# Kernel tuning notes

Hardware: AMD Instinct MI355X
Metric: run time of the kernel (lower is better)

## Reference

```python
import jax, jax.numpy as jnp
import numpy as np

N_NODES = 50000
N_EDGES = 800000
IN_C, HID_C, OUT_C = 256, 256, 128


def gcn_conv(x, W, b, row, col, n_nodes):
    """PyG GCNConv: linear transform, symmetric-normalized aggregation, bias.
    row/col already include self-loops. Messages flow row -> col."""
    h = x @ W  # [N, out]
    deg = jax.ops.segment_sum(jnp.ones_like(col, dtype=h.dtype), col, num_segments=n_nodes)
    d_inv_sqrt = jnp.where(deg > 0, jax.lax.rsqrt(jnp.maximum(deg, 1e-12)), 0.0)
    norm = d_inv_sqrt[row] * d_inv_sqrt[col]  # [E]
    msg = h[row] * norm[:, None]              # gather + scale, [E, out]
    out = jax.ops.segment_sum(msg, col, num_segments=n_nodes)  # scatter-add
    return out + b


def setup_inputs() -> dict:
    key = jax.random.key(0)
    k_x, k_e, k_w1, k_w2 = jax.random.split(key, 4)
    x = jax.random.normal(k_x, (N_NODES, IN_C), dtype=jnp.float32)
    edge_index = jax.random.randint(k_e, (2, N_EDGES), 0, N_NODES, dtype=jnp.int64)
    # Glorot-style init for GCN weights, zeros bias (PyG default)
    s1 = float(np.sqrt(6.0 / (IN_C + HID_C)))
    s2 = float(np.sqrt(6.0 / (HID_C + OUT_C)))
    W1 = jax.random.uniform(k_w1, (IN_C, HID_C), dtype=jnp.float32, minval=-s1, maxval=s1)
    b1 = jnp.zeros((HID_C,), dtype=jnp.float32)
    W2 = jax.random.uniform(k_w2, (HID_C, OUT_C), dtype=jnp.float32, minval=-s2, maxval=s2)
    b2 = jnp.zeros((OUT_C,), dtype=jnp.float32)
    return {"x": x, "edge_index": edge_index, "W1": W1, "b1": b1, "W2": W2, "b2": b2}


def reference(x, edge_index, W1, b1, W2, b2):
    n = x.shape[0]
    # add self-loops (PyG GCNConv default add_self_loops=True)
    loops = jnp.arange(n, dtype=edge_index.dtype)
    row = jnp.concatenate([edge_index[0], loops])
    col = jnp.concatenate([edge_index[1], loops])
    h = gcn_conv(x, W1, b1, row, col, n)
    h = jax.nn.relu(h)  # dropout p=0.0 -> identity
    out = gcn_conv(h, W2, b2, row, col, n)
    return out
```

## Files before the change

### kernel.cpp

```cpp
#include <hip/hip_runtime.h>

#define NN 50000
#define NE 800000
#define IN_C 256
#define HID_C 256
#define OUT_C 128

typedef unsigned short u16;
typedef __attribute__((ext_vector_type(8))) short short8;
typedef __attribute__((ext_vector_type(8))) unsigned short ushort8;
typedef __attribute__((ext_vector_type(4))) float f32x4;

__device__ __forceinline__ u16 f2b(float f) {
  unsigned int u = __float_as_uint(f);
  return (u16)((u + 0x7FFFu + ((u >> 16) & 1u)) >> 16);
}
__device__ __forceinline__ float b2f(u16 s) {
  return __uint_as_float(((unsigned int)s) << 16);
}


__global__ __launch_bounds__(256) void convw_hist(const float* __restrict__ W1,
                                                  const float* __restrict__ W2,
                                                  u16* __restrict__ W1t,
                                                  u16* __restrict__ W2t,
                                                  const int* __restrict__ col,
                                                  int* __restrict__ cnt, int E, int nhb) {
  int b = blockIdx.x;
  if (b < 256) {
    int id = b * 256 + threadIdx.x;
    int n = id >> 8, k = id & 255;
    W1t[id] = f2b(W1[k * 256 + n]);
    if (id < 128 * 256) W2t[id] = f2b(W2[k * 128 + n]);
  } else {
    int T = nhb * 256;
    int idx = (b - 256) * 256 + threadIdx.x;
#pragma unroll
    for (int i = 0; i < 8; ++i) {
      int e = idx + i * T;
      if (e < E) atomicAdd(&cnt[col[e]], 1);
    }
  }
}


__global__ __launch_bounds__(256) void scan1_kernel(const int* __restrict__ cnt,
                                                    int* __restrict__ bsum, int n) {
  __shared__ int ws[4];
  int i = blockIdx.x * 256 + threadIdx.x;
  int lane = threadIdx.x & 63, wid = threadIdx.x >> 6;
  int v = (i < n) ? cnt[i] : 0;
#pragma unroll
  for (int off = 32; off > 0; off >>= 1) v += __shfl_down(v, off, 64);
  if (lane == 0) ws[wid] = v;
  __syncthreads();
  if (threadIdx.x == 0) bsum[blockIdx.x] = ws[0] + ws[1] + ws[2] + ws[3];
}

__global__ __launch_bounds__(256) void scan23_kernel(const int* __restrict__ cnt,
                                                     const int* __restrict__ bsum,
                                                     int* __restrict__ row_off,
                                                     int* __restrict__ cursor,
                                                     float* __restrict__ dinv, int n) {
  __shared__ int ws2[4];
  __shared__ int wsum[4], wpre[4];
  int bid = blockIdx.x;
  int t = threadIdx.x;
  int lane = t & 63, wid = t >> 6;
  int bv = (t < bid) ? bsum[t] : 0;
#pragma unroll
  for (int off = 32; off > 0; off >>= 1) bv += __shfl_down(bv, off, 64);
  if (lane == 0) ws2[wid] = bv;
  __syncthreads();
  int boff = ws2[0] + ws2[1] + ws2[2] + ws2[3];
  int i = bid * 256 + t;
  int v = (i < n) ? cnt[i] : 0;
  int s = v;
#pragma unroll
  for (int off = 1; off < 64; off <<= 1) {
    int tt = __shfl_up(s, off, 64);
    if (lane >= off) s += tt;
  }
  if (lane == 63) wsum[wid] = s;
  __syncthreads();
  if (t == 0) {
    int acc = 0;
#pragma unroll
    for (int w = 0; w < 4; ++w) { wpre[w] = acc; acc += wsum[w]; }
  }
  __syncthreads();
  if (i < n) {
    int off = boff + wpre[wid] + (s - v);
    row_off[i] = off;
    cursor[i] = off;
    dinv[i] = rsqrtf((float)(v + 1));
  }
  if (bid == 0 && t == 0) row_off[n] = NE;
}


template <bool A_IS_F32>
__device__ __forceinline__ void gemm_body(const void* __restrict__ Ap,
                                          const u16* __restrict__ Bt,
                                          const float* __restrict__ dscale,
                                          u16* __restrict__ C, int M, int N,
                                          int bx, int by,
                                          u16 (&Asl)[2][5120], u16 (&Bsl)[2][5120]) {
  const int tid = threadIdx.x;
  const int row0 = by * 128;
  const int col0 = bx * 128;

  f32x4 acc[4][4] = {};

  const int seg = tid & 7;
  const int rb = tid >> 3;
  const int wave = tid >> 6, lane = tid & 63;
  const int wm = wave >> 1, wn = wave & 1;
  const int qr = lane & 15, quad = lane >> 4;

  float4 aF[4];
  ushort4 aU[4];
  ushort4 bR[4];

  auto load_tiles = [&](int k0) {
    if constexpr (A_IS_F32) {
      const float* A = (const float*)Ap;
#pragma unroll
      for (int i = 0; i < 4; ++i) {
        int gr = row0 + rb + i * 32;
        aF[i] = (gr < M) ? *(const float4*)&A[(size_t)gr * 256 + k0 + seg * 4]
                         : make_float4(0.f, 0.f, 0.f, 0.f);
      }
    } else {
      const u16* A = (const u16*)Ap;
#pragma unroll
      for (int i = 0; i < 4; ++i) {
        int gr = row0 + rb + i * 32;
        aU[i] = (gr < M) ? *(const ushort4*)&A[(size_t)gr * 256 + k0 + seg * 4]
                         : make_ushort4(0, 0, 0, 0);
      }
    }
#pragma unroll
    for (int i = 0; i < 4; ++i) {
      int n = rb + i * 32;
      bR[i] = *(const ushort4*)&Bt[(size_t)(col0 + n) * 256 + k0 + seg * 4];
    }
  };

  auto write_lds = [&](int buf) {
#pragma unroll
    for (int i = 0; i < 4; ++i) {
      int r = rb + i * 32;
      ushort4 u;
      if constexpr (A_IS_F32) {
        u.x = f2b(aF[i].x); u.y = f2b(aF[i].y);
        u.z = f2b(aF[i].z); u.w = f2b(aF[i].w);
      } else {
        u = aU[i];
      }
      *(ushort4*)&Asl[buf][r * 40 + seg * 4] = u;
      *(ushort4*)&Bsl[buf][r * 40 + seg * 4] = bR[i];
    }
  };

  load_tiles(0);
  write_lds(0);
  __syncthreads();

#pragma unroll
  for (int it = 0; it < 8; ++it) {
    const int cur = it & 1;
    if (it < 7) load_tiles((it + 1) * 32);

    short8 afr[4], bfr[4];
#pragma unroll
    for (int mt = 0; mt < 4; ++mt)
      afr[mt] = *(const short8*)&Asl[cur][(wm * 64 + mt * 16 + qr) * 40 + quad * 8];
#pragma unroll
    for (int nt = 0; nt < 4; ++nt)
      bfr[nt] = *(const short8*)&Bsl[cur][(wn * 64 + nt * 16 + qr) * 40 + quad * 8];
#pragma unroll
    for (int mt = 0; mt < 4; ++mt)
#pragma unroll
      for (int nt = 0; nt < 4; ++nt)
        acc[mt][nt] = __builtin_amdgcn_mfma_f32_16x16x32_bf16(afr[mt], bfr[nt], acc[mt][nt], 0, 0, 0);

    if (it < 7) {
      write_lds(1 - cur);
      __syncthreads();
    }
  }

#pragma unroll
  for (int mt = 0; mt < 4; ++mt) {
#pragma unroll
    for (int i = 0; i < 4; ++i) {
      int gr = row0 + wm * 64 + mt * 16 + quad * 4 + i;
      if (gr < M) {
        float sc = dscale[gr];
#pragma unroll
        for (int nt = 0; nt < 4; ++nt) {
          int gc = col0 + wn * 64 + nt * 16 + qr;
          C[(size_t)gr * N + gc] = f2b(acc[mt][nt][i] * sc);
        }
      }
    }
  }
}

template <bool A_IS_F32>
__global__ __launch_bounds__(256) void gemm_mfma(const void* __restrict__ Ap,
                                                 const u16* __restrict__ Bt,
                                                 const float* __restrict__ dscale,
                                                 u16* __restrict__ C, int M, int N) {
  __shared__ u16 Asl[2][5120];
  __shared__ u16 Bsl[2][5120];
  gemm_body<A_IS_F32>(Ap, Bt, dscale, C, M, N, blockIdx.x, blockIdx.y, Asl, Bsl);
}

__global__ __launch_bounds__(256) void gemm1_scatter(const float* __restrict__ x,
                                                     const u16* __restrict__ W1t,
                                                     const float* __restrict__ dinv,
                                                     u16* __restrict__ Hb, int M, int N,
                                                     int ngb,
                                                     const int* __restrict__ row,
                                                     const int* __restrict__ col,
                                                     int* __restrict__ cursor,
                                                     int* __restrict__ csr, int E, int nsb) {
  __shared__ u16 Asl[2][5120];
  __shared__ u16 Bsl[2][5120];
  int b = blockIdx.x;
  if (b < ngb) {
    gemm_body<true>(x, W1t, dinv, Hb, M, N, b & 1, b >> 1, Asl, Bsl);
  } else {
    int T = nsb * 256;
    int idx = (b - ngb) * 256 + threadIdx.x;
#pragma unroll
    for (int i = 0; i < 8; ++i) {
      int e = idx + i * T;
      if (e < E) {
        int c = col[e];
        int p = atomicAdd(&cursor[c], 1);
        csr[p] = row[e];
      }
    }
  }
}


__global__ __launch_bounds__(256) void agg256_bf(const u16* __restrict__ h,
                                                 const int* __restrict__ row_off,
                                                 const int* __restrict__ csr,
                                                 const float* __restrict__ dinv,
                                                 const float* __restrict__ bias,
                                                 u16* __restrict__ out, int n) {
  int wave = threadIdx.x >> 6;
  int lane = threadIdx.x & 63;
  int half = lane >> 5;
  int sl = lane & 31;
  int v = blockIdx.x * 8 + wave * 2 + half;
  if (v >= n) return;
  int beg = row_off[v], end = row_off[v + 1];
  float a[8] = {};
  int e = beg;
  for (; e < end && (e & 3); ++e) {
    int s0 = csr[e];
    ushort8 g0 = *(const ushort8*)&h[(size_t)s0 * 256 + sl * 8];
#pragma unroll
    for (int i = 0; i < 8; ++i) a[i] += b2f((u16)g0[i]);
  }
  for (; e + 7 < end; e += 8) {
    int4 i0 = *(const int4*)&csr[e];
    int4 i1 = *(const int4*)&csr[e + 4];
    int s[8] = {i0.x, i0.y, i0.z, i0.w, i1.x, i1.y, i1.z, i1.w};
    ushort8 g[8];
#pragma unroll
    for (int j = 0; j < 8; ++j)
      g[j] = *(const ushort8*)&h[(size_t)s[j] * 256 + sl * 8];
#pragma unroll
    for (int j = 0; j < 8; ++j)
#pragma unroll
      for (int i = 0; i < 8; ++i) a[i] += b2f((u16)g[j][i]);
  }
  for (; e < end; ++e) {
    int s0 = csr[e];
    ushort8 g0 = *(const ushort8*)&h[(size_t)s0 * 256 + sl * 8];
#pragma unroll
    for (int i = 0; i < 8; ++i) a[i] += b2f((u16)g0[i]);
  }
  ushort8 hs = *(const ushort8*)&h[(size_t)v * 256 + sl * 8];
#pragma unroll
  for (int i = 0; i < 8; ++i) a[i] += b2f((u16)hs[i]);
  float dv = dinv[v];
  float4 bv0 = *(const float4*)&bias[sl * 8];
  float4 bv1 = *(const float4*)&bias[sl * 8 + 4];
  float bb[8] = {bv0.x, bv0.y, bv0.z, bv0.w, bv1.x, bv1.y, bv1.z, bv1.w};
  ushort8 o;
#pragma unroll
  for (int i = 0; i < 8; ++i) {
    float r = fmaxf(a[i] * dv + bb[i], 0.f);
    o[i] = (short)f2b(r);
  }
  *(ushort8*)&out[(size_t)v * 256 + sl * 8] = o;
}

__global__ __launch_bounds__(256) void agg128_bf(const u16* __restrict__ h,
                                                 const int* __restrict__ row_off,
                                                 const int* __restrict__ csr,
                                                 const float* __restrict__ dinv,
                                                 const float* __restrict__ bias,
                                                 float* __restrict__ out, int n) {
  int wave = threadIdx.x >> 6;
  int lane = threadIdx.x & 63;
  int quarter = lane >> 4;
  int sl = lane & 15;
  int v = blockIdx.x * 16 + wave * 4 + quarter;
  if (v >= n) return;
  int beg = row_off[v], end = row_off[v + 1];
  float a[8] = {};
  int e = beg;
  for (; e < end && (e & 3); ++e) {
    int s0 = csr[e];
    ushort8 g0 = *(const ushort8*)&h[(size_t)s0 * 128 + sl * 8];
#pragma unroll
    for (int i = 0; i < 8; ++i) a[i] += b2f((u16)g0[i]);
  }
  for (; e + 7 < end; e += 8) {
    int4 i0 = *(const int4*)&csr[e];
    int4 i1 = *(const int4*)&csr[e + 4];
    int s[8] = {i0.x, i0.y, i0.z, i0.w, i1.x, i1.y, i1.z, i1.w};
    ushort8 g[8];
#pragma unroll
    for (int j = 0; j < 8; ++j)
      g[j] = *(const ushort8*)&h[(size_t)s[j] * 128 + sl * 8];
#pragma unroll
    for (int j = 0; j < 8; ++j)
#pragma unroll
      for (int i = 0; i < 8; ++i) a[i] += b2f((u16)g[j][i]);
  }
  for (; e < end; ++e) {
    int s0 = csr[e];
    ushort8 g0 = *(const ushort8*)&h[(size_t)s0 * 128 + sl * 8];
#pragma unroll
    for (int i = 0; i < 8; ++i) a[i] += b2f((u16)g0[i]);
  }
  ushort8 hs = *(const ushort8*)&h[(size_t)v * 128 + sl * 8];
#pragma unroll
  for (int i = 0; i < 8; ++i) a[i] += b2f((u16)hs[i]);
  float dv = dinv[v];
  float4 bv0 = *(const float4*)&bias[sl * 8];
  float4 bv1 = *(const float4*)&bias[sl * 8 + 4];
  float bb[8] = {bv0.x, bv0.y, bv0.z, bv0.w, bv1.x, bv1.y, bv1.z, bv1.w};
  float o[8];
#pragma unroll
  for (int i = 0; i < 8; ++i) o[i] = a[i] * dv + bb[i];
  *(float4*)&out[(size_t)v * 128 + sl * 8] = make_float4(o[0], o[1], o[2], o[3]);
  *(float4*)&out[(size_t)v * 128 + sl * 8 + 4] = make_float4(o[4], o[5], o[6], o[7]);
}


extern "C" void kernel_launch(void* const* d_in, const int* in_sizes, int n_in,
                              void* d_out, int out_size, void* d_ws, size_t ws_size,
                              hipStream_t stream) {
  const float* x = (const float*)d_in[0];
  const int* ei = (const int*)d_in[1];
  const float* W1 = (const float*)d_in[2];
  const float* b1 = (const float*)d_in[3];
  const float* W2 = (const float*)d_in[4];
  const float* b2 = (const float*)d_in[5];
  float* out = (float*)d_out;

  const int* row = ei;
  const int* col = ei + NE;

  const int NB = (NN + 255) / 256;

  u16* Hb = (u16*)d_ws;
  u16* H2b = Hb + (size_t)NN * 256;
  u16* H3b = H2b + (size_t)NN * 256;
  u16* W1t = H3b + (size_t)NN * 128;
  u16* W2t = W1t + 256 * 256;
  int* cnt = (int*)(W2t + 128 * 256);
  int* row_off = cnt + NN;
  int* cursor = row_off + NN + 4;
  float* dinv = (float*)(cursor + NN);
  int* bsum = (int*)(dinv + NN);
  int* boff_unused = bsum + 200;
  int* csr = boff_unused + 200;

  hipMemsetAsync(cnt, 0, NN * sizeof(int), stream);

  {
    const int nhb = (NE + 8 * 256 - 1) / (8 * 256);
    convw_hist<<<256 + nhb, 256, 0, stream>>>(W1, W2, W1t, W2t, col, cnt, NE, nhb);
  }

  scan1_kernel<<<NB, 256, 0, stream>>>(cnt, bsum, NN);
  scan23_kernel<<<NB, 256, 0, stream>>>(cnt, bsum, row_off, cursor, dinv, NN);

  {
    const int ngb = (HID_C / 128) * ((NN + 127) / 128);
    const int nsb = (NE + 8 * 256 - 1) / (8 * 256);
    gemm1_scatter<<<ngb + nsb, 256, 0, stream>>>(x, W1t, dinv, Hb, NN, HID_C, ngb,
                                                 row, col, cursor, csr, NE, nsb);
  }

  agg256_bf<<<(NN + 7) / 8, 256, 0, stream>>>(Hb, row_off, csr, dinv, b1, H2b, NN);

  {
    dim3 grid(OUT_C / 128, (NN + 127) / 128);
    gemm_mfma<false><<<grid, 256, 0, stream>>>(H2b, W2t, dinv, H3b, NN, OUT_C);
  }
  agg128_bf<<<(NN + 15) / 16, 256, 0, stream>>>(H3b, row_off, csr, dinv, b2, out, NN);
}
```

Before: 304.1 us.

## Fuse graph setup kernels using inter-block atomic gates instead of separate launches

Replaces the memset, histogram, two scan kernels and the GEMM1/scatter launch with two kernels. Inside each, blocks coordinate through release/acquire flag gates: counter zeroing gates the histogram, block sums gate the prefix scan, and the scan gates the CSR scatter. GEMM1 now computes its row scale directly from the degree counts, so it no longer depends on the scan. This removes kernel launch gaps and serialization, but the gates are never reset between calls, so a later call can pass them early and race. It also relies on producer blocks being scheduled before the blocks that spin on them.

```diff
diff --git a/kernel.cpp b/kernel.cpp
--- a/kernel.cpp
+++ b/kernel.cpp
@@ -5,6 +5,9 @@
 #define IN_C 256
 #define HID_C 256
 #define OUT_C 128
+#define NB 196
+#define NEB 391
+#define MAGIC 0x5EED5EED
 
 typedef unsigned short u16;
 typedef __attribute__((ext_vector_type(8))) short short8;
@@ -19,90 +22,53 @@
   return __uint_as_float(((unsigned int)s) << 16);
 }
 
-
-__global__ __launch_bounds__(256) void convw_hist(const float* __restrict__ W1,
-                                                  const float* __restrict__ W2,
-                                                  u16* __restrict__ W1t,
-                                                  u16* __restrict__ W2t,
-                                                  const int* __restrict__ col,
-                                                  int* __restrict__ cnt, int E, int nhb) {
+__device__ __forceinline__ void gate_set(int* g) {
+  __hip_atomic_store(g, MAGIC, __ATOMIC_RELEASE, __HIP_MEMORY_SCOPE_AGENT);
+}
+__device__ __forceinline__ void gate_wait(const int* g) {
+  while (__hip_atomic_load(g, __ATOMIC_ACQUIRE, __HIP_MEMORY_SCOPE_AGENT) != MAGIC) {}
+}
+
+
+__global__ __launch_bounds__(256) void k1_setup(const float* __restrict__ W1,
+                                                const float* __restrict__ W2,
+                                                u16* __restrict__ W1t,
+                                                u16* __restrict__ W2t,
+                                                const int* __restrict__ col,
+                                                int* __restrict__ cnt,
+                                                int* __restrict__ zgate) {
   int b = blockIdx.x;
+  int t = threadIdx.x;
   if (b < 256) {
-    int id = b * 256 + threadIdx.x;
+    int id = b * 256 + t;
     int n = id >> 8, k = id & 255;
     W1t[id] = f2b(W1[k * 256 + n]);
     if (id < 128 * 256) W2t[id] = f2b(W2[k * 128 + n]);
+  } else if (b < 256 + NB) {
+    int sb = b - 256;
+    int i = sb * 256 + t;
+    if (i < NN) cnt[i] = 0;
+    __threadfence();
+    __syncthreads();
+    if (t == 0) gate_set(&zgate[sb]);
   } else {
-    int T = nhb * 256;
-    int idx = (b - 256) * 256 + threadIdx.x;
+    if (t < NB) gate_wait(&zgate[t]);
+    __syncthreads();
+    const int T = NEB * 256;
+    int idx = (b - 256 - NB) * 256 + t;
 #pragma unroll
     for (int i = 0; i < 8; ++i) {
       int e = idx + i * T;
-      if (e < E) atomicAdd(&cnt[col[e]], 1);
-    }
-  }
-}
-
-
-__global__ __launch_bounds__(256) void scan1_kernel(const int* __restrict__ cnt,
-                                                    int* __restrict__ bsum, int n) {
-  __shared__ int ws[4];
-  int i = blockIdx.x * 256 + threadIdx.x;
-  int lane = threadIdx.x & 63, wid = threadIdx.x >> 6;
-  int v = (i < n) ? cnt[i] : 0;
-#pragma unroll
-  for (int off = 32; off > 0; off >>= 1) v += __shfl_down(v, off, 64);
-  if (lane == 0) ws[wid] = v;
-  __syncthreads();
-  if (threadIdx.x == 0) bsum[blockIdx.x] = ws[0] + ws[1] + ws[2] + ws[3];
-}
-
-__global__ __launch_bounds__(256) void scan23_kernel(const int* __restrict__ cnt,
-                                                     const int* __restrict__ bsum,
-                                                     int* __restrict__ row_off,
-                                                     int* __restrict__ cursor,
-                                                     float* __restrict__ dinv, int n) {
-  __shared__ int ws2[4];
-  __shared__ int wsum[4], wpre[4];
-  int bid = blockIdx.x;
-  int t = threadIdx.x;
-  int lane = t & 63, wid = t >> 6;
-  int bv = (t < bid) ? bsum[t] : 0;
-#pragma unroll
-  for (int off = 32; off > 0; off >>= 1) bv += __shfl_down(bv, off, 64);
-  if (lane == 0) ws2[wid] = bv;
-  __syncthreads();
-  int boff = ws2[0] + ws2[1] + ws2[2] + ws2[3];
-  int i = bid * 256 + t;
-  int v = (i < n) ? cnt[i] : 0;
-  int s = v;
-#pragma unroll
-  for (int off = 1; off < 64; off <<= 1) {
-    int tt = __shfl_up(s, off, 64);
-    if (lane >= off) s += tt;
-  }
-  if (lane == 63) wsum[wid] = s;
-  __syncthreads();
-  if (t == 0) {
-    int acc = 0;
-#pragma unroll
-    for (int w = 0; w < 4; ++w) { wpre[w] = acc; acc += wsum[w]; }
-  }
-  __syncthreads();
-  if (i < n) {
-    int off = boff + wpre[wid] + (s - v);
-    row_off[i] = off;
-    cursor[i] = off;
-    dinv[i] = rsqrtf((float)(v + 1));
-  }
-  if (bid == 0 && t == 0) row_off[n] = NE;
-}
-
-
-template <bool A_IS_F32>
+      if (e < NE) atomicAdd(&cnt[col[e]], 1);
+    }
+  }
+}
+
+
+template <bool A_IS_F32, bool SCALE_FROM_CNT>
 __device__ __forceinline__ void gemm_body(const void* __restrict__ Ap,
                                           const u16* __restrict__ Bt,
-                                          const float* __restrict__ dscale,
+                                          const void* __restrict__ scale_src,
                                           u16* __restrict__ C, int M, int N,
                                           int bx, int by,
                                           u16 (&Asl)[2][5120], u16 (&Bsl)[2][5120]) {
@@ -197,7 +163,11 @@
     for (int i = 0; i < 4; ++i) {
       int gr = row0 + wm * 64 + mt * 16 + quad * 4 + i;
       if (gr < M) {
-        float sc = dscale[gr];
+        float sc;
+        if constexpr (SCALE_FROM_CNT)
+          sc = rsqrtf((float)(((const int*)scale_src)[gr] + 1));
+        else
+          sc = ((const float*)scale_src)[gr];
 #pragma unroll
         for (int nt = 0; nt < 4; ++nt) {
           int gc = col0 + wn * 64 + nt * 16 + qr;
@@ -208,43 +178,89 @@
   }
 }
 
-template <bool A_IS_F32>
-__global__ __launch_bounds__(256) void gemm_mfma(const void* __restrict__ Ap,
-                                                 const u16* __restrict__ Bt,
-                                                 const float* __restrict__ dscale,
-                                                 u16* __restrict__ C, int M, int N) {
-  __shared__ u16 Asl[2][5120];
-  __shared__ u16 Bsl[2][5120];
-  gemm_body<A_IS_F32>(Ap, Bt, dscale, C, M, N, blockIdx.x, blockIdx.y, Asl, Bsl);
-}
-
-__global__ __launch_bounds__(256) void gemm1_scatter(const float* __restrict__ x,
-                                                     const u16* __restrict__ W1t,
-                                                     const float* __restrict__ dinv,
-                                                     u16* __restrict__ Hb, int M, int N,
-                                                     int ngb,
-                                                     const int* __restrict__ row,
-                                                     const int* __restrict__ col,
-                                                     int* __restrict__ cursor,
-                                                     int* __restrict__ csr, int E, int nsb) {
+
+__global__ __launch_bounds__(256) void k2_scan_scatter_gemm1(
+    const int* __restrict__ cnt, int* __restrict__ bsum, int* __restrict__ sgate,
+    int* __restrict__ row_off, int* __restrict__ cursor, float* __restrict__ dinv,
+    int* __restrict__ cgate, const int* __restrict__ row, const int* __restrict__ col,
+    int* __restrict__ csr, const float* __restrict__ x, const u16* __restrict__ W1t,
+    u16* __restrict__ Hb) {
   __shared__ u16 Asl[2][5120];
   __shared__ u16 Bsl[2][5120];
   int b = blockIdx.x;
-  if (b < ngb) {
-    gemm_body<true>(x, W1t, dinv, Hb, M, N, b & 1, b >> 1, Asl, Bsl);
-  } else {
-    int T = nsb * 256;
-    int idx = (b - ngb) * 256 + threadIdx.x;
+  int t = threadIdx.x;
+  if (b < NB) {
+    __shared__ int wsum[4], wpre[5], ws2[4];
+    int lane = t & 63, wid = t >> 6;
+    int i = b * 256 + t;
+    int v = (i < NN) ? cnt[i] : 0;
+    int s = v;
+#pragma unroll
+    for (int off = 1; off < 64; off <<= 1) {
+      int tt = __shfl_up(s, off, 64);
+      if (lane >= off) s += tt;
+    }
+    if (lane == 63) wsum[wid] = s;
+    __syncthreads();
+    if (t == 0) {
+      int acc = 0;
+#pragma unroll
+      for (int w = 0; w < 4; ++w) { wpre[w] = acc; acc += wsum[w]; }
+      wpre[4] = acc;
+    }
+    __syncthreads();
+    if (t == 0) {
+      bsum[b] = wpre[4];
+      __threadfence();
+      gate_set(&sgate[b]);
+    }
+    int bv = 0;
+    if (t < b) {
+      gate_wait(&sgate[t]);
+      bv = bsum[t];
+    }
+#pragma unroll
+    for (int off = 32; off > 0; off >>= 1) bv += __shfl_down(bv, off, 64);
+    if (lane == 0) ws2[wid] = bv;
+    __syncthreads();
+    int boffs = ws2[0] + ws2[1] + ws2[2] + ws2[3];
+    if (i < NN) {
+      int off = boffs + wpre[wid] + (s - v);
+      row_off[i] = off;
+      cursor[i] = off;
+      dinv[i] = rsqrtf((float)(v + 1));
+    }
+    if (b == 0 && t == 0) row_off[NN] = NE;
+    __threadfence();
+    __syncthreads();
+    if (t == 0) gate_set(&cgate[b]);
+  } else if (b < NB + NEB) {
+    if (t < NB) gate_wait(&cgate[t]);
+    __syncthreads();
+    const int T = NEB * 256;
+    int idx = (b - NB) * 256 + t;
 #pragma unroll
     for (int i = 0; i < 8; ++i) {
       int e = idx + i * T;
-      if (e < E) {
+      if (e < NE) {
         int c = col[e];
         int p = atomicAdd(&cursor[c], 1);
-        csr[p] = row[e];
+        __builtin_nontemporal_store(row[e], &csr[p]);
       }
     }
-  }
+  } else {
+    int gb = b - NB - NEB;
+    gemm_body<true, true>(x, W1t, cnt, Hb, NN, HID_C, gb & 1, gb >> 1, Asl, Bsl);
+  }
+}
+
+__global__ __launch_bounds__(256) void gemm_mfma2(const u16* __restrict__ Ap,
+                                                  const u16* __restrict__ Bt,
+                                                  const float* __restrict__ dinv,
+                                                  u16* __restrict__ C, int M, int N) {
+  __shared__ u16 Asl[2][5120];
+  __shared__ u16 Bsl[2][5120];
+  gemm_body<false, false>(Ap, Bt, dinv, C, M, N, blockIdx.x, blockIdx.y, Asl, Bsl);
 }
 
 
@@ -373,8 +389,6 @@
   const int* row = ei;
   const int* col = ei + NE;
 
-  const int NB = (NN + 255) / 256;
-
   u16* Hb = (u16*)d_ws;
   u16* H2b = Hb + (size_t)NN * 256;
   u16* H3b = H2b + (size_t)NN * 256;
@@ -385,31 +399,22 @@
   int* cursor = row_off + NN + 4;
   float* dinv = (float*)(cursor + NN);
   int* bsum = (int*)(dinv + NN);
-  int* boff_unused = bsum + 200;
-  int* csr = boff_unused + 200;
-
-  hipMemsetAsync(cnt, 0, NN * sizeof(int), stream);
-
-  {
-    const int nhb = (NE + 8 * 256 - 1) / (8 * 256);
-    convw_hist<<<256 + nhb, 256, 0, stream>>>(W1, W2, W1t, W2t, col, cnt, NE, nhb);
-  }
-
-  scan1_kernel<<<NB, 256, 0, stream>>>(cnt, bsum, NN);
-  scan23_kernel<<<NB, 256, 0, stream>>>(cnt, bsum, row_off, cursor, dinv, NN);
-
-  {
-    const int ngb = (HID_C / 128) * ((NN + 127) / 128);
-    const int nsb = (NE + 8 * 256 - 1) / (8 * 256);
-    gemm1_scatter<<<ngb + nsb, 256, 0, stream>>>(x, W1t, dinv, Hb, NN, HID_C, ngb,
-                                                 row, col, cursor, csr, NE, nsb);
-  }
+  int* zgate = bsum + 256;
+  int* sgate = zgate + 256;
+  int* cgate = sgate + 256;
+  int* csr = cgate + 256;
+
+  k1_setup<<<256 + NB + NEB, 256, 0, stream>>>(W1, W2, W1t, W2t, col, cnt, zgate);
+
+  k2_scan_scatter_gemm1<<<NB + NEB + 782, 256, 0, stream>>>(
+      cnt, bsum, sgate, row_off, cursor, dinv, cgate, row, col, csr, x, W1t, Hb);
 
   agg256_bf<<<(NN + 7) / 8, 256, 0, stream>>>(Hb, row_off, csr, dinv, b1, H2b, NN);
 
   {
     dim3 grid(OUT_C / 128, (NN + 127) / 128);
-    gemm_mfma<false><<<grid, 256, 0, stream>>>(H2b, W2t, dinv, H3b, NN, OUT_C);
-  }
+    gemm_mfma2<<<grid, 256, 0, stream>>>(H2b, W2t, dinv, H3b, NN, OUT_C);
+  }
+
   agg128_bf<<<(NN + 15) / 16, 256, 0, stream>>>(H3b, row_off, csr, dinv, b2, out, NN);
 }
```

New measurement: 461.8 us. +51.9%, slower.

## Fuse all GCN stages into one cooperative persistent kernel with grid syncs

Applied to the files above, without the earlier changes.

Replaces the sequence of eight launches (memset, histogram, two scan passes, GEMM+scatter, aggregation, GEMM, aggregation) with a single cooperative kernel of 768 blocks. Stages are separated by grid-wide barriers, and each stage's blocks loop over its work items. The aim is to remove per-launch overhead and the idle gaps between dependent kernels. The trade-off is that every stage is capped at a fixed grid with 3 blocks per CU, the grid barriers have their own cost, and the GEMM tiles now run at lower concurrency. The CSR scatter stores also become nontemporal, and the old multi-kernel path is kept as a fallback if the cooperative launch fails.

```diff
diff --git a/kernel.cpp b/kernel.cpp
--- a/kernel.cpp
+++ b/kernel.cpp
@@ -1,10 +1,18 @@
 #include <hip/hip_runtime.h>
+#include <hip/hip_cooperative_groups.h>
+
+namespace cg = cooperative_groups;
 
 #define NN 50000
 #define NE 800000
 #define IN_C 256
 #define HID_C 256
 #define OUT_C 128
+#define NB 196
+#define NEB 391
+#define G1TILES 782
+#define G2TILES 391
+#define GRID 768
 
 typedef unsigned short u16;
 typedef __attribute__((ext_vector_type(8))) short short8;
@@ -17,85 +25,6 @@
 }
 __device__ __forceinline__ float b2f(u16 s) {
   return __uint_as_float(((unsigned int)s) << 16);
-}
-
-
-__global__ __launch_bounds__(256) void convw_hist(const float* __restrict__ W1,
-                                                  const float* __restrict__ W2,
-                                                  u16* __restrict__ W1t,
-                                                  u16* __restrict__ W2t,
-                                                  const int* __restrict__ col,
-                                                  int* __restrict__ cnt, int E, int nhb) {
-  int b = blockIdx.x;
-  if (b < 256) {
-    int id = b * 256 + threadIdx.x;
-    int n = id >> 8, k = id & 255;
-    W1t[id] = f2b(W1[k * 256 + n]);
-    if (id < 128 * 256) W2t[id] = f2b(W2[k * 128 + n]);
-  } else {
-    int T = nhb * 256;
-    int idx = (b - 256) * 256 + threadIdx.x;
-#pragma unroll
-    for (int i = 0; i < 8; ++i) {
-      int e = idx + i * T;
-      if (e < E) atomicAdd(&cnt[col[e]], 1);
-    }
-  }
-}
-
-
-__global__ __launch_bounds__(256) void scan1_kernel(const int* __restrict__ cnt,
-                                                    int* __restrict__ bsum, int n) {
-  __shared__ int ws[4];
-  int i = blockIdx.x * 256 + threadIdx.x;
-  int lane = threadIdx.x & 63, wid = threadIdx.x >> 6;
-  int v = (i < n) ? cnt[i] : 0;
-#pragma unroll
-  for (int off = 32; off > 0; off >>= 1) v += __shfl_down(v, off, 64);
-  if (lane == 0) ws[wid] = v;
-  __syncthreads();
-  if (threadIdx.x == 0) bsum[blockIdx.x] = ws[0] + ws[1] + ws[2] + ws[3];
-}
-
-__global__ __launch_bounds__(256) void scan23_kernel(const int* __restrict__ cnt,
-                                                     const int* __restrict__ bsum,
-                                                     int* __restrict__ row_off,
-                                                     int* __restrict__ cursor,
-                                                     float* __restrict__ dinv, int n) {
-  __shared__ int ws2[4];
-  __shared__ int wsum[4], wpre[4];
-  int bid = blockIdx.x;
-  int t = threadIdx.x;
-  int lane = t & 63, wid = t >> 6;
-  int bv = (t < bid) ? bsum[t] : 0;
-#pragma unroll
-  for (int off = 32; off > 0; off >>= 1) bv += __shfl_down(bv, off, 64);
-  if (lane == 0) ws2[wid] = bv;
-  __syncthreads();
-  int boff = ws2[0] + ws2[1] + ws2[2] + ws2[3];
-  int i = bid * 256 + t;
-  int v = (i < n) ? cnt[i] : 0;
-  int s = v;
-#pragma unroll
-  for (int off = 1; off < 64; off <<= 1) {
-    int tt = __shfl_up(s, off, 64);
-    if (lane >= off) s += tt;
-  }
-  if (lane == 63) wsum[wid] = s;
-  __syncthreads();
-  if (t == 0) {
-    int acc = 0;
-#pragma unroll
-    for (int w = 0; w < 4; ++w) { wpre[w] = acc; acc += wsum[w]; }
-  }
-  __syncthreads();
-  if (i < n) {
-    int off = boff + wpre[wid] + (s - v);
-    row_off[i] = off;
-    cursor[i] = off;
-    dinv[i] = rsqrtf((float)(v + 1));
-  }
-  if (bid == 0 && t == 0) row_off[n] = NE;
 }
 
 
@@ -208,58 +137,19 @@
   }
 }
 
-template <bool A_IS_F32>
-__global__ __launch_bounds__(256) void gemm_mfma(const void* __restrict__ Ap,
-                                                 const u16* __restrict__ Bt,
-                                                 const float* __restrict__ dscale,
-                                                 u16* __restrict__ C, int M, int N) {
-  __shared__ u16 Asl[2][5120];
-  __shared__ u16 Bsl[2][5120];
-  gemm_body<A_IS_F32>(Ap, Bt, dscale, C, M, N, blockIdx.x, blockIdx.y, Asl, Bsl);
-}
-
-__global__ __launch_bounds__(256) void gemm1_scatter(const float* __restrict__ x,
-                                                     const u16* __restrict__ W1t,
-                                                     const float* __restrict__ dinv,
-                                                     u16* __restrict__ Hb, int M, int N,
-                                                     int ngb,
-                                                     const int* __restrict__ row,
-                                                     const int* __restrict__ col,
-                                                     int* __restrict__ cursor,
-                                                     int* __restrict__ csr, int E, int nsb) {
-  __shared__ u16 Asl[2][5120];
-  __shared__ u16 Bsl[2][5120];
-  int b = blockIdx.x;
-  if (b < ngb) {
-    gemm_body<true>(x, W1t, dinv, Hb, M, N, b & 1, b >> 1, Asl, Bsl);
-  } else {
-    int T = nsb * 256;
-    int idx = (b - ngb) * 256 + threadIdx.x;
-#pragma unroll
-    for (int i = 0; i < 8; ++i) {
-      int e = idx + i * T;
-      if (e < E) {
-        int c = col[e];
-        int p = atomicAdd(&cursor[c], 1);
-        csr[p] = row[e];
-      }
-    }
-  }
-}
-
-
-__global__ __launch_bounds__(256) void agg256_bf(const u16* __restrict__ h,
-                                                 const int* __restrict__ row_off,
-                                                 const int* __restrict__ csr,
-                                                 const float* __restrict__ dinv,
-                                                 const float* __restrict__ bias,
-                                                 u16* __restrict__ out, int n) {
+
+__device__ __forceinline__ void agg256_body(int blk, const u16* __restrict__ h,
+                                            const int* __restrict__ row_off,
+                                            const int* __restrict__ csr,
+                                            const float* __restrict__ dinv,
+                                            const float* __restrict__ bias,
+                                            u16* __restrict__ out) {
   int wave = threadIdx.x >> 6;
   int lane = threadIdx.x & 63;
   int half = lane >> 5;
   int sl = lane & 31;
-  int v = blockIdx.x * 8 + wave * 2 + half;
-  if (v >= n) return;
+  int v = blk * 8 + wave * 2 + half;
+  if (v >= NN) return;
   int beg = row_off[v], end = row_off[v + 1];
   float a[8] = {};
   int e = beg;
@@ -304,18 +194,18 @@
   *(ushort8*)&out[(size_t)v * 256 + sl * 8] = o;
 }
 
-__global__ __launch_bounds__(256) void agg128_bf(const u16* __restrict__ h,
-                                                 const int* __restrict__ row_off,
-                                                 const int* __restrict__ csr,
-                                                 const float* __restrict__ dinv,
-                                                 const float* __restrict__ bias,
-                                                 float* __restrict__ out, int n) {
+__device__ __forceinline__ void agg128_body(int blk, const u16* __restrict__ h,
+                                            const int* __restrict__ row_off,
+                                            const int* __restrict__ csr,
+                                            const float* __restrict__ dinv,
+                                            const float* __restrict__ bias,
+                                            float* __restrict__ out) {
   int wave = threadIdx.x >> 6;
   int lane = threadIdx.x & 63;
   int quarter = lane >> 4;
   int sl = lane & 15;
-  int v = blockIdx.x * 16 + wave * 4 + quarter;
-  if (v >= n) return;
+  int v = blk * 16 + wave * 4 + quarter;
+  if (v >= NN) return;
   int beg = row_off[v], end = row_off[v + 1];
   float a[8] = {};
   int e = beg;
@@ -356,6 +246,249 @@
   for (int i = 0; i < 8; ++i) o[i] = a[i] * dv + bb[i];
   *(float4*)&out[(size_t)v * 128 + sl * 8] = make_float4(o[0], o[1], o[2], o[3]);
   *(float4*)&out[(size_t)v * 128 + sl * 8 + 4] = make_float4(o[4], o[5], o[6], o[7]);
+}
+
+
+struct MegaParams {
+  const float* W1; const float* W2;
+  u16* W1t; u16* W2t;
+  const int* row; const int* col;
+  int* cnt; int* bsum; int* row_off; int* cursor; float* dinv; int* csr;
+  const float* x; u16* Hb;
+  const float* b1; u16* H2b;
+  u16* H3b;
+  const float* b2; float* out;
+};
+
+__global__ __launch_bounds__(256, 3) void mega(MegaParams p) {
+  cg::grid_group grid = cg::this_grid();
+  __shared__ u16 Asl[2][5120];
+  __shared__ u16 Bsl[2][5120];
+  __shared__ int sA[4], sB[5], sC[4];
+  const int b = blockIdx.x;
+  const int t = threadIdx.x;
+  const int lane = t & 63, wid = t >> 6;
+
+  if (b < 256) {
+    int id = b * 256 + t;
+    int n = id >> 8, k = id & 255;
+    p.W1t[id] = f2b(p.W1[k * 256 + n]);
+    if (id < 128 * 256) p.W2t[id] = f2b(p.W2[k * 128 + n]);
+  } else if (b < 256 + NB) {
+    int i = (b - 256) * 256 + t;
+    if (i < NN) p.cnt[i] = 0;
+  }
+  grid.sync();
+
+  for (int e = b * 256 + t; e < NE; e += GRID * 256)
+    atomicAdd(&p.cnt[p.col[e]], 1);
+  grid.sync();
+
+  if (b < NB) {
+    int i = b * 256 + t;
+    int v = (i < NN) ? p.cnt[i] : 0;
+#pragma unroll
+    for (int off = 32; off > 0; off >>= 1) v += __shfl_down(v, off, 64);
+    if (lane == 0) sA[wid] = v;
+    __syncthreads();
+    if (t == 0) p.bsum[b] = sA[0] + sA[1] + sA[2] + sA[3];
+  }
+  grid.sync();
+
+  if (b < NB) {
+    int bv = (t < b) ? p.bsum[t] : 0;
+#pragma unroll
+    for (int off = 32; off > 0; off >>= 1) bv += __shfl_down(bv, off, 64);
+    if (lane == 0) sC[wid] = bv;
+    __syncthreads();
+    int boffs = sC[0] + sC[1] + sC[2] + sC[3];
+    int i = b * 256 + t;
+    int v = (i < NN) ? p.cnt[i] : 0;
+    int s = v;
+#pragma unroll
+    for (int off = 1; off < 64; off <<= 1) {
+      int tt = __shfl_up(s, off, 64);
+      if (lane >= off) s += tt;
+    }
+    if (lane == 63) sA[wid] = s;
+    __syncthreads();
+    if (t == 0) {
+      int acc = 0;
+#pragma unroll
+      for (int w = 0; w < 4; ++w) { sB[w] = acc; acc += sA[w]; }
+    }
+    __syncthreads();
+    if (i < NN) {
+      int off = boffs + sB[wid] + (s - v);
+      p.row_off[i] = off;
+      p.cursor[i] = off;
+      p.dinv[i] = rsqrtf((float)(v + 1));
+    }
+    if (b == 0 && t == 0) p.row_off[NN] = NE;
+  }
+  grid.sync();
+
+  for (int u = b; u < NEB + G1TILES; u += GRID) {
+    if (u < NEB) {
+      const int T = NEB * 256;
+      int idx = u * 256 + t;
+#pragma unroll
+      for (int i = 0; i < 8; ++i) {
+        int e = idx + i * T;
+        if (e < NE) {
+          int c = p.col[e];
+          int pos = atomicAdd(&p.cursor[c], 1);
+          __builtin_nontemporal_store(p.row[e], &p.csr[pos]);
+        }
+      }
+    } else {
+      int gb = u - NEB;
+      gemm_body<true>(p.x, p.W1t, p.dinv, p.Hb, NN, HID_C, gb & 1, gb >> 1, Asl, Bsl);
+    }
+  }
+  grid.sync();
+
+  for (int u = b; u < (NN + 7) / 8; u += GRID)
+    agg256_body(u, p.Hb, p.row_off, p.csr, p.dinv, p.b1, p.H2b);
+  grid.sync();
+
+  for (int u = b; u < G2TILES; u += GRID)
+    gemm_body<false>(p.H2b, p.W2t, p.dinv, p.H3b, NN, OUT_C, 0, u, Asl, Bsl);
+  grid.sync();
+
+  for (int u = b; u < (NN + 15) / 16; u += GRID)
+    agg128_body(u, p.H3b, p.row_off, p.csr, p.dinv, p.b2, p.out);
+}
+
+
+__global__ __launch_bounds__(256) void convw_hist(const float* __restrict__ W1,
+                                                  const float* __restrict__ W2,
+                                                  u16* __restrict__ W1t,
+                                                  u16* __restrict__ W2t,
+                                                  const int* __restrict__ col,
+                                                  int* __restrict__ cnt) {
+  int b = blockIdx.x;
+  if (b < 256) {
+    int id = b * 256 + threadIdx.x;
+    int n = id >> 8, k = id & 255;
+    W1t[id] = f2b(W1[k * 256 + n]);
+    if (id < 128 * 256) W2t[id] = f2b(W2[k * 128 + n]);
+  } else {
+    const int T = NEB * 256;
+    int idx = (b - 256) * 256 + threadIdx.x;
+#pragma unroll
+    for (int i = 0; i < 8; ++i) {
+      int e = idx + i * T;
+      if (e < NE) atomicAdd(&cnt[col[e]], 1);
+    }
+  }
+}
+
+__global__ __launch_bounds__(256) void scan1_kernel(const int* __restrict__ cnt,
+                                                    int* __restrict__ bsum) {
+  __shared__ int ws[4];
+  int i = blockIdx.x * 256 + threadIdx.x;
+  int lane = threadIdx.x & 63, wid = threadIdx.x >> 6;
+  int v = (i < NN) ? cnt[i] : 0;
+#pragma unroll
+  for (int off = 32; off > 0; off >>= 1) v += __shfl_down(v, off, 64);
+  if (lane == 0) ws[wid] = v;
+  __syncthreads();
+  if (threadIdx.x == 0) bsum[blockIdx.x] = ws[0] + ws[1] + ws[2] + ws[3];
+}
+
+__global__ __launch_bounds__(256) void scan23_kernel(const int* __restrict__ cnt,
+                                                     const int* __restrict__ bsum,
+                                                     int* __restrict__ row_off,
+                                                     int* __restrict__ cursor,
+                                                     float* __restrict__ dinv) {
+  __shared__ int ws2[4], wsum[4], wpre[4];
+  int b = blockIdx.x, t = threadIdx.x;
+  int lane = t & 63, wid = t >> 6;
+  int bv = (t < b) ? bsum[t] : 0;
+#pragma unroll
+  for (int off = 32; off > 0; off >>= 1) bv += __shfl_down(bv, off, 64);
+  if (lane == 0) ws2[wid] = bv;
+  __syncthreads();
+  int boffs = ws2[0] + ws2[1] + ws2[2] + ws2[3];
+  int i = b * 256 + t;
+  int v = (i < NN) ? cnt[i] : 0;
+  int s = v;
+#pragma unroll
+  for (int off = 1; off < 64; off <<= 1) {
+    int tt = __shfl_up(s, off, 64);
+    if (lane >= off) s += tt;
+  }
+  if (lane == 63) wsum[wid] = s;
+  __syncthreads();
+  if (t == 0) {
+    int acc = 0;
+#pragma unroll
+    for (int w = 0; w < 4; ++w) { wpre[w] = acc; acc += wsum[w]; }
+  }
+  __syncthreads();
+  if (i < NN) {
+    int off = boffs + wpre[wid] + (s - v);
+    row_off[i] = off;
+    cursor[i] = off;
+    dinv[i] = rsqrtf((float)(v + 1));
+  }
+  if (b == 0 && t == 0) row_off[NN] = NE;
+}
+
+__global__ __launch_bounds__(256) void gemm1_scatter(const float* __restrict__ x,
+                                                     const u16* __restrict__ W1t,
+                                                     const float* __restrict__ dinv,
+                                                     u16* __restrict__ Hb, int ngb,
+                                                     const int* __restrict__ row,
+                                                     const int* __restrict__ col,
+                                                     int* __restrict__ cursor,
+                                                     int* __restrict__ csr) {
+  __shared__ u16 Asl[2][5120];
+  __shared__ u16 Bsl[2][5120];
+  int b = blockIdx.x;
+  if (b < ngb) {
+    gemm_body<true>(x, W1t, dinv, Hb, NN, HID_C, b & 1, b >> 1, Asl, Bsl);
+  } else {
+    const int T = NEB * 256;
+    int idx = (b - ngb) * 256 + threadIdx.x;
+#pragma unroll
+    for (int i = 0; i < 8; ++i) {
+      int e = idx + i * T;
+      if (e < NE) {
+        int c = col[e];
+        int p = atomicAdd(&cursor[c], 1);
+        __builtin_nontemporal_store(row[e], &csr[p]);
+      }
+    }
+  }
+}
+
+__global__ __launch_bounds__(256) void gemm_mfma2(const u16* __restrict__ Ap,
+                                                  const u16* __restrict__ Bt,
+                                                  const float* __restrict__ dinv,
+                                                  u16* __restrict__ C) {
+  __shared__ u16 Asl[2][5120];
+  __shared__ u16 Bsl[2][5120];
+  gemm_body<false>(Ap, Bt, dinv, C, NN, OUT_C, blockIdx.x, blockIdx.y, Asl, Bsl);
+}
+
+__global__ __launch_bounds__(256) void agg256_bf(const u16* __restrict__ h,
+                                                 const int* __restrict__ row_off,
+                                                 const int* __restrict__ csr,
+                                                 const float* __restrict__ dinv,
+                                                 const float* __restrict__ bias,
+                                                 u16* __restrict__ out) {
+  agg256_body(blockIdx.x, h, row_off, csr, dinv, bias, out);
+}
+
+__global__ __launch_bounds__(256) void agg128_bf(const u16* __restrict__ h,
+                                                 const int* __restrict__ row_off,
+                                                 const int* __restrict__ csr,
+                                                 const float* __restrict__ dinv,
+                                                 const float* __restrict__ bias,
+                                                 float* __restrict__ out) {
+  agg128_body(blockIdx.x, h, row_off, csr, dinv, bias, out);
 }
 
 
@@ -373,8 +506,6 @@
   const int* row = ei;
   const int* col = ei + NE;
 
-  const int NB = (NN + 255) / 256;
-
   u16* Hb = (u16*)d_ws;
   u16* H2b = Hb + (size_t)NN * 256;
   u16* H3b = H2b + (size_t)NN * 256;
@@ -385,31 +516,31 @@
   int* cursor = row_off + NN + 4;
   float* dinv = (float*)(cursor + NN);
   int* bsum = (int*)(dinv + NN);
-  int* boff_unused = bsum + 200;
-  int* csr = boff_unused + 200;
-
-  hipMemsetAsync(cnt, 0, NN * sizeof(int), stream);
-
-  {
-    const int nhb = (NE + 8 * 256 - 1) / (8 * 256);
-    convw_hist<<<256 + nhb, 256, 0, stream>>>(W1, W2, W1t, W2t, col, cnt, NE, nhb);
-  }
-
-  scan1_kernel<<<NB, 256, 0, stream>>>(cnt, bsum, NN);
-  scan23_kernel<<<NB, 256, 0, stream>>>(cnt, bsum, row_off, cursor, dinv, NN);
-
-  {
-    const int ngb = (HID_C / 128) * ((NN + 127) / 128);
-    const int nsb = (NE + 8 * 256 - 1) / (8 * 256);
-    gemm1_scatter<<<ngb + nsb, 256, 0, stream>>>(x, W1t, dinv, Hb, NN, HID_C, ngb,
-                                                 row, col, cursor, csr, NE, nsb);
-  }
-
-  agg256_bf<<<(NN + 7) / 8, 256, 0, stream>>>(Hb, row_off, csr, dinv, b1, H2b, NN);
-
-  {
-    dim3 grid(OUT_C / 128, (NN + 127) / 128);
-    gemm_mfma<false><<<grid, 256, 0, stream>>>(H2b, W2t, dinv, H3b, NN, OUT_C);
-  }
-  agg128_bf<<<(NN + 15) / 16, 256, 0, stream>>>(H3b, row_off, csr, dinv, b2, out, NN);
-}
+  int* csr = bsum + 256;
+
+  MegaParams p;
+  p.W1 = W1; p.W2 = W2; p.W1t = W1t; p.W2t = W2t;
+  p.row = row; p.col = col;
+  p.cnt = cnt; p.bsum = bsum; p.row_off = row_off; p.cursor = cursor;
+  p.dinv = dinv; p.csr = csr;
+  p.x = x; p.Hb = Hb; p.b1 = b1; p.H2b = H2b; p.H3b = H3b; p.b2 = b2; p.out = out;
+
+  void* args[] = {(void*)&p};
+  hipError_t err = hipLaunchCooperativeKernel((const void*)mega, dim3(GRID), dim3(256),
+                                              args, 0, stream);
+  if (err != hipSuccess) {
+    (void)hipGetLastError();
+    hipMemsetAsync(cnt, 0, NN * sizeof(int), stream);
+    convw_hist<<<256 + NEB, 256, 0, stream>>>(W1, W2, W1t, W2t, col, cnt);
+    scan1_kernel<<<NB, 256, 0, stream>>>(cnt, bsum);
+    scan23_kernel<<<NB, 256, 0, stream>>>(cnt, bsum, row_off, cursor, dinv);
+    gemm1_scatter<<<G1TILES + NEB, 256, 0, stream>>>(x, W1t, dinv, Hb, G1TILES,
+                                                     row, col, cursor, csr);
+    agg256_bf<<<(NN + 7) / 8, 256, 0, stream>>>(Hb, row_off, csr, dinv, b1, H2b);
+    {
+      dim3 grid(OUT_C / 128, (NN + 127) / 128);
+      gemm_mfma2<<<grid, 256, 0, stream>>>(H2b, W2t, dinv, H3b);
+    }
+    agg128_bf<<<(NN + 15) / 16, 256, 0, stream>>>(H3b, row_off, csr, dinv, b2, out);
+  }
+}
```

New measurement: 964.6 us. 217% more time.
